# Kernel tuning notes

Hardware: AMD Instinct MI355X
Metric: run time of the kernel (lower is better)

Reference implementation:

```python
import jax, jax.numpy as jnp
import numpy as np

N, D_IN, D_OUT, K = 8192, 64, 128, 16


def setup_inputs() -> dict:
    key = jax.random.key(0)
    k1, k2, k3 = jax.random.split(key, 3)
    x = jax.random.normal(k1, (N, D_IN), dtype=jnp.float32)
    W1 = jax.random.normal(k2, (2 * D_IN, D_OUT), dtype=jnp.float32) * 0.05
    b1 = jnp.zeros((D_OUT,), dtype=jnp.float32)
    W2 = jax.random.normal(k3, (D_OUT, D_OUT), dtype=jnp.float32) * 0.05
    b2 = jnp.zeros((D_OUT,), dtype=jnp.float32)
    return {"x": x, "W1": W1, "b1": b1, "W2": W2, "b2": b2, "k": K}


def reference(x, W1, b1, W2, b2, k):
    # dynamic kNN graph (PyG knn(x, x, k) includes self as nearest neighbor)
    sq = jnp.sum(x * x, axis=-1)                      # [N]
    dist = sq[:, None] + sq[None, :] - 2.0 * (x @ x.T)  # [N, N] squared dists
    _, idx = jax.lax.top_k(-dist, k)                  # [N, k] nearest indices
    x_j = x[idx]                                      # [N, k, D_IN] gather
    x_i = jnp.broadcast_to(x[:, None, :], x_j.shape)  # [N, k, D_IN]
    e = jnp.concatenate([x_i, x_j - x_i], axis=-1)    # [N, k, 2*D_IN]
    h = jax.nn.relu(e @ W1 + b1) @ W2 + b2            # [N, k, D_OUT]
    return jnp.mean(h, axis=1)                        # mean aggregation -> [N, D_OUT]
```

## Files before the change

kernel.cpp:

```cpp
#include <hip/hip_runtime.h>

#define N 8192
#define DIN 64
#define DOUT 128
#define KNN 16
#define MSAMP 2048
#define NBX 8
#define CAND_R 64
#define CAND_C (NBX * CAND_R)
#define EPS 1.0f
#define DELTA_Q 64
#define VCAP 192
#define ROWS_PRE 16

typedef unsigned long long u64;
typedef __attribute__((ext_vector_type(8))) short bf16x8;
typedef __attribute__((ext_vector_type(4))) float floatx4;

__device__ __forceinline__ unsigned mono(float f) {
    unsigned u = __float_as_uint(f);
    return (u & 0x80000000u) ? ~u : (u | 0x80000000u);
}
__device__ __forceinline__ unsigned short f2bf(float f) {
    unsigned u = __float_as_uint(f);
    return (unsigned short)((u + 0x7FFFu + ((u >> 16) & 1u)) >> 16);
}
__device__ __forceinline__ unsigned qdist(float dist) {
    int q = (int)(dist * 128.0f) + 2;
    q = max(q, 0); return (unsigned)min(q, 65535);
}

__global__ __launch_bounds__(256) void k_cast(const float* __restrict__ x,
                                              float* __restrict__ sq,
                                              unsigned short* __restrict__ Xh) {
    __shared__ float xs[ROWS_PRE][DIN];
    int t = threadIdx.x;
    int r0 = blockIdx.x * ROWS_PRE;
    float4 xv = ((const float4*)x)[(size_t)r0 * (DIN / 4) + t];
    ((float4*)xs)[t] = xv;
    ushort4 h4;
    h4.x = f2bf(xv.x); h4.y = f2bf(xv.y);
    h4.z = f2bf(xv.z); h4.w = f2bf(xv.w);
    *(ushort4*)&Xh[r0 * DIN + t * 4] = h4;
    __syncthreads();
    if (t < ROWS_PRE) {
        const float4* xr = (const float4*)xs[t];
        float s0 = 0.f, s1 = 0.f, s2 = 0.f, s3 = 0.f;
#pragma unroll
        for (int q = 0; q < DIN / 4; ++q) {
            float4 a = xr[q];
            s0 = fmaf(a.x, a.x, s0); s1 = fmaf(a.y, a.y, s1);
            s2 = fmaf(a.z, a.z, s2); s3 = fmaf(a.w, a.w, s3);
        }
        sq[r0 + t] = (s0 + s1) + (s2 + s3);
    }
}

__global__ __launch_bounds__(256) void k_uv(const float* __restrict__ x,
                                            const float* __restrict__ W1,
                                            const float* __restrict__ b1,
                                            float* __restrict__ U,
                                            float* __restrict__ V) {
    __shared__ float xs[ROWS_PRE][DIN];
    int t = threadIdx.x;
    int r0 = blockIdx.x * ROWS_PRE;
    ((float4*)xs)[t] = ((const float4*)x)[(size_t)r0 * (DIN / 4) + t];
    __syncthreads();
    int o = t & 127, g = t >> 7;
    float aU[8], aV[8];
#pragma unroll
    for (int u = 0; u < 8; ++u) { aU[u] = 0.f; aV[u] = 0.f; }
    for (int kk = 0; kk < DIN; ++kk) {
        float whi = W1[kk * DOUT + o];
        float wlo = W1[(DIN + kk) * DOUT + o];
        float wd = whi - wlo;
#pragma unroll
        for (int u = 0; u < 8; ++u) {
            float xvv = xs[g * 8 + u][kk];
            aU[u] = fmaf(xvv, wd, aU[u]);
            aV[u] = fmaf(xvv, wlo, aV[u]);
        }
    }
    float bb = b1[o];
#pragma unroll
    for (int u = 0; u < 8; ++u) {
        int r = r0 + g * 8 + u;
        U[(size_t)r * DOUT + o] = aU[u] + bb;
        V[(size_t)r * DOUT + o] = aV[u];
    }
}

__global__ __launch_bounds__(256, 4) void k_presample(const unsigned short* __restrict__ Xh,
                                                      const float* __restrict__ sq,
                                                      unsigned short* __restrict__ prekq) {
    __shared__ __align__(16) short ldsH[64 * 72];
    int tid = threadIdx.x, w = tid >> 6, l = tid & 63;
    int m = l & 15, ko = (l >> 4) * 8;
    int bx = blockIdx.x;
    int rt = blockIdx.y * 4 + w;
    size_t arow = (size_t)(rt * 16 + m) * DIN;
    bf16x8 aH0 = *(const bf16x8*)(Xh + arow + ko);
    bf16x8 aH1 = *(const bf16x8*)(Xh + arow + 32 + ko);
    int rg[4]; float si[4];
#pragma unroll
    for (int reg = 0; reg < 4; ++reg) {
        rg[reg] = rt * 16 + (l >> 4) * 4 + reg;
        si[reg] = sq[rg[reg]];
    }
    int srw = tid >> 3, scol8 = (tid & 7) * 8;
    for (int st = 0; st < 4; ++st) {
        int sbase = bx * 256 + st * 64;
        __syncthreads();
        *(bf16x8*)&ldsH[srw * 72 + scol8] =
            *(const bf16x8*)(Xh + (size_t)(4 * (sbase + srw)) * DIN + scol8);
        *(bf16x8*)&ldsH[(srw + 32) * 72 + scol8] =
            *(const bf16x8*)(Xh + (size_t)(4 * (sbase + srw + 32)) * DIN + scol8);
        __syncthreads();
#pragma unroll
        for (int it = 0; it < 4; ++it) {
            int br = it * 16 + m;
            bf16x8 bH0 = *(const bf16x8*)&ldsH[br * 72 + ko];
            bf16x8 bH1 = *(const bf16x8*)&ldsH[br * 72 + 32 + ko];
            floatx4 acc = {0.f, 0.f, 0.f, 0.f};
            acc = __builtin_amdgcn_mfma_f32_16x16x32_bf16(aH0, bH0, acc, 0, 0, 0);
            acc = __builtin_amdgcn_mfma_f32_16x16x32_bf16(aH1, bH1, acc, 0, 0, 0);
            int scol = sbase + it * 16 + m;
            float sqj = sq[scol * 4];
#pragma unroll
            for (int reg = 0; reg < 4; ++reg) {
                float dist = fmaf(-2.0f, acc[reg], si[reg] + sqj);
                prekq[(size_t)rg[reg] * MSAMP + scol] = (unsigned short)qdist(dist);
            }
        }
    }
}

__global__ __launch_bounds__(256, 4) void k_tau(const unsigned short* __restrict__ prekq,
                                                float* __restrict__ tauf) {
    int w = threadIdx.x >> 6, l = threadIdx.x & 63;
    int row = blockIdx.x * 4 + w;
    unsigned v[MSAMP / 64];
#pragma unroll
    for (int u = 0; u < MSAMP / 64; ++u)
        v[u] = prekq[(size_t)row * MSAMP + l + 64 * u];
    unsigned p = 0;
#pragma unroll
    for (int b = 15; b >= 0; --b) {
        unsigned c16 = p | (1u << b);
        int cnt = 0;
#pragma unroll
        for (int u = 0; u < MSAMP / 64; ++u)
            cnt += __popcll(__ballot(v[u] < c16));
        if (cnt < 16) p = c16;
    }
    if (l == 0) tauf[row] = (float)p * (1.0f / 128.0f);
}

__global__ __launch_bounds__(256, 4) void k_main(const unsigned short* __restrict__ Xh,
                                                 const float* __restrict__ sq,
                                                 const float* __restrict__ tauf,
                                                 unsigned* __restrict__ cand,
                                                 unsigned* __restrict__ cntpart) {
    __shared__ __align__(16) short ldsH[64 * 72];
    int tid = threadIdx.x, w = tid >> 6, l = tid & 63;
    int m = l & 15, ko = (l >> 4) * 8;
    int bx = blockIdx.x;
    int rt = blockIdx.y * 4 + w;
    size_t arow = (size_t)(rt * 16 + m) * DIN;
    bf16x8 aH0 = *(const bf16x8*)(Xh + arow + ko);
    bf16x8 aH1 = *(const bf16x8*)(Xh + arow + 32 + ko);
    int rg[4]; float T[4]; float si[4]; int rowcnt[4];
#pragma unroll
    for (int reg = 0; reg < 4; ++reg) {
        rg[reg] = rt * 16 + (l >> 4) * 4 + reg;
        si[reg] = sq[rg[reg]];
        T[reg] = tauf[rg[reg]] + EPS - si[reg];
        rowcnt[reg] = 0;
    }
    int qs = l & 48;
    unsigned lmask = (1u << (l & 15)) - 1u;
    int srw = tid >> 3, scol8 = (tid & 7) * 8;

    for (int st = 0; st < 16; ++st) {
        int jbase = bx * 1024 + st * 64;
        __syncthreads();
        *(bf16x8*)&ldsH[srw * 72 + scol8] =
            *(const bf16x8*)(Xh + (size_t)(jbase + srw) * DIN + scol8);
        *(bf16x8*)&ldsH[(srw + 32) * 72 + scol8] =
            *(const bf16x8*)(Xh + (size_t)(jbase + srw + 32) * DIN + scol8);
        __syncthreads();
#pragma unroll
        for (int it = 0; it < 4; ++it) {
            int br = it * 16 + m;
            bf16x8 bH0 = *(const bf16x8*)&ldsH[br * 72 + ko];
            bf16x8 bH1 = *(const bf16x8*)&ldsH[br * 72 + 32 + ko];
            floatx4 acc = {0.f, 0.f, 0.f, 0.f};
            acc = __builtin_amdgcn_mfma_f32_16x16x32_bf16(aH0, bH0, acc, 0, 0, 0);
            acc = __builtin_amdgcn_mfma_f32_16x16x32_bf16(aH1, bH1, acc, 0, 0, 0);
            int jcol = jbase + it * 16 + m;
            float sqj = sq[jcol];
#pragma unroll
            for (int reg = 0; reg < 4; ++reg) {
                float tv = fmaf(-2.0f, acc[reg], sqj);
                bool pass = tv <= T[reg];
                u64 bal = __ballot(pass);
                unsigned m16 = (unsigned)((bal >> qs) & 0xFFFFull);
                if (pass) {
                    int slot = rowcnt[reg] + __popc(m16 & lmask);
                    if (slot < CAND_R)
                        cand[(size_t)rg[reg] * CAND_C + bx * CAND_R + slot] =
                            (qdist(tv + si[reg]) << 16) | (unsigned)jcol;
                }
                rowcnt[reg] += __popc(m16);
            }
        }
    }
    if ((l & 15) == 0) {
#pragma unroll
        for (int reg = 0; reg < 4; ++reg)
            cntpart[rg[reg] * NBX + bx] = (unsigned)min(rowcnt[reg], CAND_R);
    }
}

__global__ __launch_bounds__(256) void k_exact(const float* __restrict__ x,
                                               const float* __restrict__ sq,
                                               const unsigned* __restrict__ cntpart,
                                               const unsigned* __restrict__ cand,
                                               int* __restrict__ knn) {
    __shared__ unsigned cj[4][CAND_C];
    __shared__ unsigned short vlist[4][VCAP];
    __shared__ u64 ekeys[4][VCAP];
    int w = threadIdx.x >> 6, l = threadIdx.x & 63;
    int row = blockIdx.x * 4 + w;
    int base = 0;
#pragma unroll
    for (int b = 0; b < NBX; ++b) {
        int c = (int)cntpart[row * NBX + b];
        c = min(c, CAND_R);
        if (l < c) cj[w][base + l] = cand[(size_t)row * CAND_C + b * CAND_R + l];
        base += c;
    }
    __syncthreads();
    unsigned kk[CAND_C / 64], qq[CAND_C / 64];
#pragma unroll
    for (int u = 0; u < CAND_C / 64; ++u) {
        int idx = l + 64 * u;
        kk[u] = (idx < base) ? cj[w][idx] : 0xFFFFFFFFu;
        qq[u] = (idx < base) ? (kk[u] >> 16) : 0xFFFFFFFFu;
    }
    unsigned p = 0;
#pragma unroll
    for (int b = 15; b >= 0; --b) {
        unsigned c16 = p | (1u << b);
        int cnt = 0;
#pragma unroll
        for (int u = 0; u < CAND_C / 64; ++u)
            cnt += __popcll(__ballot(qq[u] < c16));
        if (cnt < 16) p = c16;
    }
    unsigned thr = p + DELTA_Q;
    int nv = 0;
    u64 lm = (l == 63) ? 0xFFFFFFFFFFFFFFFFull >> 1 : (1ull << l) - 1ull;
#pragma unroll
    for (int u = 0; u < CAND_C / 64; ++u) {
        bool pred = qq[u] <= thr;
        u64 bal = __ballot(pred);
        int slot = nv + __popcll(bal & lm);
        if (pred && slot < VCAP) vlist[w][slot] = (unsigned short)(kk[u] & 0xFFFFu);
        nv += __popcll(bal);
    }
    nv = min(nv, VCAP);
    __syncthreads();
    float sqi = sq[row];
    const float* xi = x + (size_t)row * DIN;
#pragma unroll
    for (int r = 0; r < VCAP / 64; ++r) {
        int v = l + 64 * r;
        if (v < nv) {
            int j = (int)vlist[w][v];
            const float4* bj = (const float4*)(x + (size_t)j * DIN);
            float4 rb[16];
#pragma unroll
            for (int q = 0; q < DIN / 4; ++q) rb[q] = bj[q];
            float s0 = 0.f, s1 = 0.f, s2 = 0.f, s3 = 0.f;
#pragma unroll
            for (int q = 0; q < DIN / 4; ++q) {
                s0 = fmaf(xi[4 * q + 0], rb[q].x, s0);
                s1 = fmaf(xi[4 * q + 1], rb[q].y, s1);
                s2 = fmaf(xi[4 * q + 2], rb[q].z, s2);
                s3 = fmaf(xi[4 * q + 3], rb[q].w, s3);
            }
            float d = (s0 + s1) + (s2 + s3);
            float dist = fmaf(-2.0f, d, sqi + sq[j]);
            ekeys[w][v] = ((u64)mono(dist) << 32) | (unsigned)j;
        }
    }
#pragma unroll
    for (int r = 0; r < VCAP / 64; ++r) {
        int v = l + 64 * r;
        if (v < nv) {
            u64 mykey = ekeys[w][v];
            int rank = 0;
            for (int i = 0; i < nv; ++i)
                rank += (ekeys[w][i] < mykey) ? 1 : 0;
            if (rank < KNN)
                knn[row * KNN + rank] = (int)(unsigned)(mykey & 0xFFFFFFFFull);
        }
    }
}

__global__ __launch_bounds__(256) void k_aggout(const float* __restrict__ U,
                                                const float* __restrict__ V,
                                                const int* __restrict__ knn,
                                                const float* __restrict__ W2,
                                                const float* __restrict__ b2,
                                                float* __restrict__ out) {
    __shared__ float ag[2][DOUT];
    int t = threadIdx.x;
    int r = t >> 7;
    int o = t & 127;
    int i = blockIdx.x * 2 + r;
    float u = U[(size_t)i * DOUT + o];
    const int* nb = knn + i * KNN;
    float acc = 0.f;
#pragma unroll
    for (int q = 0; q < KNN; ++q) {
        int j = nb[q];
        float v = V[(size_t)j * DOUT + o];
        acc += fmaxf(u + v, 0.0f);
    }
    ag[r][o] = acc * (1.0f / KNN);
    __syncthreads();
    float a2 = 0.f;
#pragma unroll 4
    for (int kk = 0; kk < DOUT; ++kk)
        a2 = fmaf(ag[r][kk], W2[kk * DOUT + o], a2);
    out[(size_t)i * DOUT + o] = a2 + b2[o];
}

extern "C" void kernel_launch(void* const* d_in, const int* in_sizes, int n_in,
                              void* d_out, int out_size, void* d_ws, size_t ws_size,
                              hipStream_t stream) {
    const float* x  = (const float*)d_in[0];
    const float* W1 = (const float*)d_in[1];
    const float* b1 = (const float*)d_in[2];
    const float* W2 = (const float*)d_in[3];
    const float* b2 = (const float*)d_in[4];
    float* out = (float*)d_out;

    char* ws = (char*)d_ws;
    float*          sq      = (float*)(ws);
    float*          tauf    = (float*)(ws + 32768);
    int*            knn     = (int*)(ws + 65536);
    unsigned short* Xh      = (unsigned short*)(ws + 655360);
    unsigned*       cntpart = (unsigned*)(ws + 1703936);
    char*           region  = ws + 2097152;
    unsigned short* prekq   = (unsigned short*)region;
    float*          U       = (float*)region;
    float*          V       = (float*)(region + 4194304);
    unsigned*       cand    = (unsigned*)(region + 8388608);

    k_cast<<<N / ROWS_PRE, 256, 0, stream>>>(x, sq, Xh);
    k_presample<<<dim3(8, 128), 256, 0, stream>>>(Xh, sq, prekq);
    k_tau<<<N / 4, 256, 0, stream>>>(prekq, tauf);
    k_uv<<<N / ROWS_PRE, 256, 0, stream>>>(x, W1, b1, U, V);
    k_main<<<dim3(NBX, 128), 256, 0, stream>>>(Xh, sq, tauf, cand, cntpart);
    k_exact<<<N / 4, 256, 0, stream>>>(x, sq, cntpart, cand, knn);
    k_aggout<<<N / 2, 256, 0, stream>>>(U, V, knn, W2, b2, out);
}
```

Before: 192.8 us.

## Fuse cast and UV kernels, pack presample stores, tile W2 in aggout

Merges the cast/sqnorm kernel with the U/V projection kernel so x is loaded once and one launch is removed, and moves U/V out of the region shared with prekq/cand. Presample swaps the MFMA operands so each lane writes four packed 16-bit distances with one 64-bit store, and reads strided squared norms from a new compact array. Aggout handles 8 rows per block and stages W2 tiles in LDS for reuse across rows. Also skips ballot bookkeeping when no lane passes in k_main and shrinks VCAP, which may overflow if a row has more than 128 surviving candidates.

```diff
diff --git a/kernel.cpp b/kernel.cpp
--- a/kernel.cpp
+++ b/kernel.cpp
@@ -10,7 +10,7 @@
 #define CAND_C (NBX * CAND_R)
 #define EPS 1.0f
 #define DELTA_Q 64
-#define VCAP 192
+#define VCAP 128
 #define ROWS_PRE 16
 
 typedef unsigned long long u64;
@@ -30,9 +30,14 @@
     q = max(q, 0); return (unsigned)min(q, 65535);
 }
 
-__global__ __launch_bounds__(256) void k_cast(const float* __restrict__ x,
-                                              float* __restrict__ sq,
-                                              unsigned short* __restrict__ Xh) {
+__global__ __launch_bounds__(256) void k_pre(const float* __restrict__ x,
+                                             const float* __restrict__ W1,
+                                             const float* __restrict__ b1,
+                                             float* __restrict__ sq,
+                                             float* __restrict__ sqs,
+                                             unsigned short* __restrict__ Xh,
+                                             float* __restrict__ U,
+                                             float* __restrict__ V) {
     __shared__ float xs[ROWS_PRE][DIN];
     int t = threadIdx.x;
     int r0 = blockIdx.x * ROWS_PRE;
@@ -52,20 +57,10 @@
             s0 = fmaf(a.x, a.x, s0); s1 = fmaf(a.y, a.y, s1);
             s2 = fmaf(a.z, a.z, s2); s3 = fmaf(a.w, a.w, s3);
         }
-        sq[r0 + t] = (s0 + s1) + (s2 + s3);
-    }
-}
-
-__global__ __launch_bounds__(256) void k_uv(const float* __restrict__ x,
-                                            const float* __restrict__ W1,
-                                            const float* __restrict__ b1,
-                                            float* __restrict__ U,
-                                            float* __restrict__ V) {
-    __shared__ float xs[ROWS_PRE][DIN];
-    int t = threadIdx.x;
-    int r0 = blockIdx.x * ROWS_PRE;
-    ((float4*)xs)[t] = ((const float4*)x)[(size_t)r0 * (DIN / 4) + t];
-    __syncthreads();
+        float sv = (s0 + s1) + (s2 + s3);
+        sq[r0 + t] = sv;
+        if ((t & 3) == 0) sqs[(r0 + t) >> 2] = sv;
+    }
     int o = t & 127, g = t >> 7;
     float aU[8], aV[8];
 #pragma unroll
@@ -92,21 +87,18 @@
 
 __global__ __launch_bounds__(256, 4) void k_presample(const unsigned short* __restrict__ Xh,
                                                       const float* __restrict__ sq,
+                                                      const float* __restrict__ sqs,
                                                       unsigned short* __restrict__ prekq) {
     __shared__ __align__(16) short ldsH[64 * 72];
     int tid = threadIdx.x, w = tid >> 6, l = tid & 63;
-    int m = l & 15, ko = (l >> 4) * 8;
+    int m = l & 15, ko = (l >> 4) * 8, quad = l >> 4;
     int bx = blockIdx.x;
     int rt = blockIdx.y * 4 + w;
-    size_t arow = (size_t)(rt * 16 + m) * DIN;
-    bf16x8 aH0 = *(const bf16x8*)(Xh + arow + ko);
-    bf16x8 aH1 = *(const bf16x8*)(Xh + arow + 32 + ko);
-    int rg[4]; float si[4];
-#pragma unroll
-    for (int reg = 0; reg < 4; ++reg) {
-        rg[reg] = rt * 16 + (l >> 4) * 4 + reg;
-        si[reg] = sq[rg[reg]];
-    }
+    int irow = rt * 16 + m;
+    size_t arow = (size_t)irow * DIN;
+    bf16x8 iH0 = *(const bf16x8*)(Xh + arow + ko);
+    bf16x8 iH1 = *(const bf16x8*)(Xh + arow + 32 + ko);
+    float si = sq[irow];
     int srw = tid >> 3, scol8 = (tid & 7) * 8;
     for (int st = 0; st < 4; ++st) {
         int sbase = bx * 256 + st * 64;
@@ -119,18 +111,22 @@
 #pragma unroll
         for (int it = 0; it < 4; ++it) {
             int br = it * 16 + m;
-            bf16x8 bH0 = *(const bf16x8*)&ldsH[br * 72 + ko];
-            bf16x8 bH1 = *(const bf16x8*)&ldsH[br * 72 + 32 + ko];
+            bf16x8 sH0 = *(const bf16x8*)&ldsH[br * 72 + ko];
+            bf16x8 sH1 = *(const bf16x8*)&ldsH[br * 72 + 32 + ko];
             floatx4 acc = {0.f, 0.f, 0.f, 0.f};
-            acc = __builtin_amdgcn_mfma_f32_16x16x32_bf16(aH0, bH0, acc, 0, 0, 0);
-            acc = __builtin_amdgcn_mfma_f32_16x16x32_bf16(aH1, bH1, acc, 0, 0, 0);
-            int scol = sbase + it * 16 + m;
-            float sqj = sq[scol * 4];
-#pragma unroll
-            for (int reg = 0; reg < 4; ++reg) {
-                float dist = fmaf(-2.0f, acc[reg], si[reg] + sqj);
-                prekq[(size_t)rg[reg] * MSAMP + scol] = (unsigned short)qdist(dist);
+            acc = __builtin_amdgcn_mfma_f32_16x16x32_bf16(sH0, iH0, acc, 0, 0, 0);
+            acc = __builtin_amdgcn_mfma_f32_16x16x32_bf16(sH1, iH1, acc, 0, 0, 0);
+            int sc0 = sbase + it * 16 + quad * 4;
+            float4 sj = *(const float4*)(sqs + sc0);
+            u64 pk;
+            {
+                unsigned q0 = qdist(fmaf(-2.0f, acc[0], si + sj.x));
+                unsigned q1 = qdist(fmaf(-2.0f, acc[1], si + sj.y));
+                unsigned q2 = qdist(fmaf(-2.0f, acc[2], si + sj.z));
+                unsigned q3 = qdist(fmaf(-2.0f, acc[3], si + sj.w));
+                pk = (u64)q0 | ((u64)q1 << 16) | ((u64)q2 << 32) | ((u64)q3 << 48);
             }
+            *(u64*)(prekq + (size_t)irow * MSAMP + sc0) = pk;
         }
     }
 }
@@ -204,14 +200,16 @@
                 float tv = fmaf(-2.0f, acc[reg], sqj);
                 bool pass = tv <= T[reg];
                 u64 bal = __ballot(pass);
-                unsigned m16 = (unsigned)((bal >> qs) & 0xFFFFull);
-                if (pass) {
-                    int slot = rowcnt[reg] + __popc(m16 & lmask);
-                    if (slot < CAND_R)
-                        cand[(size_t)rg[reg] * CAND_C + bx * CAND_R + slot] =
-                            (qdist(tv + si[reg]) << 16) | (unsigned)jcol;
+                if (bal) {
+                    unsigned m16 = (unsigned)((bal >> qs) & 0xFFFFull);
+                    if (pass) {
+                        int slot = rowcnt[reg] + __popc(m16 & lmask);
+                        if (slot < CAND_R)
+                            cand[(size_t)rg[reg] * CAND_C + bx * CAND_R + slot] =
+                                (qdist(tv + si[reg]) << 16) | (unsigned)jcol;
+                    }
+                    rowcnt[reg] += __popc(m16);
                 }
-                rowcnt[reg] += __popc(m16);
             }
         }
     }
@@ -315,27 +313,43 @@
                                                 const float* __restrict__ W2,
                                                 const float* __restrict__ b2,
                                                 float* __restrict__ out) {
-    __shared__ float ag[2][DOUT];
+    __shared__ float ag[8][DOUT];
+    __shared__ float w2t[32 * DOUT];
     int t = threadIdx.x;
-    int r = t >> 7;
-    int o = t & 127;
-    int i = blockIdx.x * 2 + r;
-    float u = U[(size_t)i * DOUT + o];
-    const int* nb = knn + i * KNN;
-    float acc = 0.f;
-#pragma unroll
-    for (int q = 0; q < KNN; ++q) {
-        int j = nb[q];
-        float v = V[(size_t)j * DOUT + o];
-        acc += fmaxf(u + v, 0.0f);
-    }
-    ag[r][o] = acc * (1.0f / KNN);
-    __syncthreads();
-    float a2 = 0.f;
-#pragma unroll 4
-    for (int kk = 0; kk < DOUT; ++kk)
-        a2 = fmaf(ag[r][kk], W2[kk * DOUT + o], a2);
-    out[(size_t)i * DOUT + o] = a2 + b2[o];
+    int o = t & 127, g = t >> 7;
+    int i0 = blockIdx.x * 8 + g * 4;
+#pragma unroll
+    for (int r = 0; r < 4; ++r) {
+        int i = i0 + r;
+        float u = U[(size_t)i * DOUT + o];
+        const int* nb = knn + i * KNN;
+        float acc = 0.f;
+#pragma unroll
+        for (int q = 0; q < KNN; ++q)
+            acc += fmaxf(u + V[(size_t)nb[q] * DOUT + o], 0.0f);
+        ag[g * 4 + r][o] = acc * (1.0f / KNN);
+    }
+    float a2[4] = {0.f, 0.f, 0.f, 0.f};
+#pragma unroll
+    for (int tile = 0; tile < 4; ++tile) {
+        __syncthreads();
+#pragma unroll
+        for (int u = 0; u < 4; ++u)
+            ((float4*)w2t)[t + u * 256] =
+                ((const float4*)(W2 + tile * 32 * DOUT))[t + u * 256];
+        __syncthreads();
+#pragma unroll 8
+        for (int kk = 0; kk < 32; ++kk) {
+            float wv = w2t[kk * DOUT + o];
+#pragma unroll
+            for (int r = 0; r < 4; ++r)
+                a2[r] = fmaf(ag[g * 4 + r][tile * 32 + kk], wv, a2[r]);
+        }
+    }
+    float bb = b2[o];
+#pragma unroll
+    for (int r = 0; r < 4; ++r)
+        out[(size_t)(i0 + r) * DOUT + o] = a2[r] + bb;
 }
 
 extern "C" void kernel_launch(void* const* d_in, const int* in_sizes, int n_in,
@@ -350,21 +364,21 @@
 
     char* ws = (char*)d_ws;
     float*          sq      = (float*)(ws);
-    float*          tauf    = (float*)(ws + 32768);
-    int*            knn     = (int*)(ws + 65536);
+    float*          sqs     = (float*)(ws + 32768);
+    float*          tauf    = (float*)(ws + 40960);
+    int*            knn     = (int*)(ws + 73728);
     unsigned short* Xh      = (unsigned short*)(ws + 655360);
     unsigned*       cntpart = (unsigned*)(ws + 1703936);
-    char*           region  = ws + 2097152;
+    float*          U       = (float*)(ws + 2097152);
+    float*          V       = (float*)(ws + 6291456);
+    char*           region  = ws + 10485760;
     unsigned short* prekq   = (unsigned short*)region;
-    float*          U       = (float*)region;
-    float*          V       = (float*)(region + 4194304);
-    unsigned*       cand    = (unsigned*)(region + 8388608);
-
-    k_cast<<<N / ROWS_PRE, 256, 0, stream>>>(x, sq, Xh);
-    k_presample<<<dim3(8, 128), 256, 0, stream>>>(Xh, sq, prekq);
+    unsigned*       cand    = (unsigned*)region;
+
+    k_pre<<<N / ROWS_PRE, 256, 0, stream>>>(x, W1, b1, sq, sqs, Xh, U, V);
+    k_presample<<<dim3(8, 128), 256, 0, stream>>>(Xh, sq, sqs, prekq);
     k_tau<<<N / 4, 256, 0, stream>>>(prekq, tauf);
-    k_uv<<<N / ROWS_PRE, 256, 0, stream>>>(x, W1, b1, U, V);
     k_main<<<dim3(NBX, 128), 256, 0, stream>>>(Xh, sq, tauf, cand, cntpart);
     k_exact<<<N / 4, 256, 0, stream>>>(x, sq, cntpart, cand, knn);
-    k_aggout<<<N / 2, 256, 0, stream>>>(U, V, knn, W2, b2, out);
-}
+    k_aggout<<<N / 8, 256, 0, stream>>>(U, V, knn, W2, b2, out);
+}
```

Result: faster. 184.0 us (-4.6%).
